# Kernel tuning notes

Hardware: AMD Instinct MI355X
Metric: run time of the kernel (lower is better)

Reference implementation:

```python
import jax, jax.numpy as jnp
import numpy as np
from jax import lax

C = 256          # fpn_feats_dim
NC = 20          # num_classes
GROUPS = 16      # GroupNorm groups
EPS = 1e-5       # GroupNorm eps (torch default)
BATCH = 8
LEVELS = [(100, 128), (50, 64), (25, 32)]  # FPN level H,W for 800x1024 image, strides 8/16/32
PRIOR_BIAS = -float(np.log((1 - 0.01) / 0.01))  # ~-4.5951, FCOS prior init


def _conv3(x, w, b):
    # 3x3 stride-1 pad-1 conv, NCHW / OIHW
    y = lax.conv_general_dilated(x, w, (1, 1), 'SAME',
                                 dimension_numbers=('NCHW', 'OIHW', 'NCHW'))
    return y + b[None, :, None, None]


def _gn(x, g, b):
    n, c, h, w = x.shape
    xr = x.reshape(n, GROUPS, c // GROUPS, h, w)
    m = xr.mean(axis=(2, 3, 4), keepdims=True)
    v = xr.var(axis=(2, 3, 4), keepdims=True)
    xr = (xr - m) * lax.rsqrt(v + EPS)
    x = xr.reshape(n, c, h, w)
    return x * g[None, :, None, None] + b[None, :, None, None]


def _forward(feat0, feat1, feat2,
             cls_conv_w, cls_conv_b, cls_gn_g, cls_gn_b, cls_out_w, cls_out_b,
             reg_conv_w, reg_conv_b, reg_gn_g, reg_gn_b,
             reg_out_w, reg_out_b, ctr_w, ctr_b):
    feats = [feat0, feat1, feat2]
    all_cls, all_reg, all_ctr = [], [], []
    for f in feats:
        n = f.shape[0]
        x = f
        for i in range(2):
            x = jax.nn.relu(_gn(_conv3(x, cls_conv_w[i], cls_conv_b[i]),
                                cls_gn_g[i], cls_gn_b[i]))
        logits = _conv3(x, cls_out_w, cls_out_b)           # [N, NC, H, W]
        # view(N,-1,NC,H,W).permute(0,3,4,1,2).reshape(N,-1,NC) == NHWC flatten
        all_cls.append(logits.transpose(0, 2, 3, 1).reshape(n, -1, NC))
        t = f
        for i in range(2):
            t = jax.nn.relu(_gn(_conv3(t, reg_conv_w[i], reg_conv_b[i]),
                                reg_gn_g[i], reg_gn_b[i]))
        # bbox_reg = Sequential(conv, ReLU), then an extra relu in forward (idempotent)
        bbox = jax.nn.relu(jax.nn.relu(_conv3(t, reg_out_w, reg_out_b)))  # [N,4,H,W]
        all_reg.append(bbox.transpose(0, 2, 3, 1).reshape(n, -1, 1))      # [N,H*W*4,1]
        ctr = _conv3(t, ctr_w, ctr_b)                                     # [N,1,H,W]
        all_ctr.append(ctr.transpose(0, 2, 3, 1).reshape(n, -1, 1))       # [N,H*W,1]
    cls_cat = jnp.concatenate(all_cls, axis=1)
    reg_cat = jnp.concatenate(all_reg, axis=1)
    ctr_cat = jnp.concatenate(all_ctr, axis=1)
    return cls_cat, reg_cat, ctr_cat


def setup_inputs() -> dict:
    key = jax.random.key(0)
    ks = jax.random.split(key, 20)
    std = 0.01
    d = {}
    for i, (h, w) in enumerate(LEVELS):
        d[f"feat{i}"] = jax.random.normal(ks[i], (BATCH, C, h, w), jnp.float32)
    # classification head params
    d["cls_conv_w"] = jax.random.normal(ks[3], (2, C, C, 3, 3), jnp.float32) * std
    d["cls_conv_b"] = jnp.zeros((2, C), jnp.float32)
    d["cls_gn_g"] = jnp.ones((2, C), jnp.float32)
    d["cls_gn_b"] = jnp.zeros((2, C), jnp.float32)
    d["cls_out_w"] = jax.random.normal(ks[4], (NC, C, 3, 3), jnp.float32) * std
    d["cls_out_b"] = jnp.full((NC,), PRIOR_BIAS, jnp.float32)
    d["reg_conv_w"] = jax.random.normal(ks[5], (2, C, C, 3, 3), jnp.float32) * std
    d["reg_conv_b"] = jnp.zeros((2, C), jnp.float32)
    d["reg_gn_g"] = jnp.ones((2, C), jnp.float32)
    d["reg_gn_b"] = jnp.zeros((2, C), jnp.float32)
    d["reg_out_w"] = jax.random.normal(ks[6], (4, C, 3, 3), jnp.float32) * std
    d["reg_out_b"] = jnp.zeros((4,), jnp.float32)
    d["ctr_w"] = jax.random.normal(ks[7], (1, C, 3, 3), jnp.float32) * std
    d["ctr_b"] = jnp.zeros((1,), jnp.float32)
    return d


def reference(feat0, feat1, feat2,
              cls_conv_w, cls_conv_b, cls_gn_g, cls_gn_b, cls_out_w, cls_out_b,
              reg_conv_w, reg_conv_b, reg_gn_g, reg_gn_b,
              reg_out_w, reg_out_b, ctr_w, ctr_b):
    return _forward(feat0, feat1, feat2,
                    cls_conv_w, cls_conv_b, cls_gn_g, cls_gn_b, cls_out_w, cls_out_b,
                    reg_conv_w, reg_conv_b, reg_gn_g, reg_gn_b,
                    reg_out_w, reg_out_b, ctr_w, ctr_b)
```

## Files before the change

kernel.cpp:

```cpp
#include <hip/hip_runtime.h>

typedef unsigned short u16;
typedef __attribute__((ext_vector_type(8))) unsigned short ushort8v;
typedef __attribute__((ext_vector_type(8))) short short8v;
typedef __attribute__((ext_vector_type(4))) float floatx4;

__device__ __forceinline__ float bf2f(u16 u) {
    unsigned v = ((unsigned)u) << 16;
    float f;
    __builtin_memcpy(&f, &v, 4);
    return f;
}
__device__ __forceinline__ u16 f2bf(float f) {
    unsigned v;
    __builtin_memcpy(&v, &f, 4);
    unsigned r = (v + 0x7fffu + ((v >> 16) & 1u)) >> 16;
    return (u16)r;
}
__device__ __forceinline__ float ld(const void* p, long i, int isf) {
    return isf ? ((const float*)p)[i] : bf2f(((const u16*)p)[i]);
}
__device__ __forceinline__ void gll16(const void* g, void* l) {
    __builtin_amdgcn_global_load_lds(
        (const __attribute__((address_space(1))) unsigned int*)g,
        (__attribute__((address_space(3))) unsigned int*)l, 16, 0, 0);
}

__global__ void detect_dtype(const u16* __restrict__ gng, int* __restrict__ flag) {
    if (threadIdx.x == 0) flag[0] = (gng[0] == 0x3F80u) ? 0 : 1;
}

__global__ void conv_params(const void* ccb, const void* cgg, const void* cgb,
                            const void* rcb, const void* rgg, const void* rgb,
                            const void* cob, const void* rob, const void* ctb,
                            const int* __restrict__ flag, u16* __restrict__ dst) {
    const int isf = flag[0];
    for (int i = threadIdx.x; i < 3104; i += 256) {
        const void* src; int off;
        if (i < 512)       { src = ccb; off = i; }
        else if (i < 1024) { src = cgg; off = i - 512; }
        else if (i < 1536) { src = cgb; off = i - 1024; }
        else if (i < 2048) { src = rcb; off = i - 1536; }
        else if (i < 2560) { src = rgg; off = i - 2048; }
        else if (i < 3072) { src = rgb; off = i - 2560; }
        else if (i < 3092) { src = cob; off = i - 3072; }
        else if (i < 3096) { src = rob; off = i - 3092; }
        else if (i < 3097) { src = ctb; off = 0; }
        else               { dst[i] = 0; continue; }
        dst[i] = f2bf(ld(src, off, isf));
    }
}

__global__ void prep_w(const void* __restrict__ src, long srcOff,
                       const int* __restrict__ flag, u16* __restrict__ dst,
                       int CoutSrc, int BNr) {
    const int isf = flag[0];
    unsigned e = blockIdx.x * 256 + threadIdx.x;
    unsigned c = e & 31u;
    unsigned r = (e >> 5) % (unsigned)BNr;
    unsigned kc = (e / (32u * BNr)) % 72u;
    unsigned nt = e / (32u * BNr * 72u);
    unsigned co = nt * BNr + r;
    unsigned tap = kc >> 3, ci = (kc & 7u) * 32u + c;
    u16 v = 0;
    if (co < (unsigned)CoutSrc)
        v = f2bf(ld(src, srcOff + (long)(co * 256u + ci) * 9 + tap, isf));
    dst[e] = v;
}

__global__ void prep_w_regctr(const void* __restrict__ wreg, const void* __restrict__ wctr,
                              const int* __restrict__ flag, u16* __restrict__ dst) {
    const int isf = flag[0];
    unsigned e = blockIdx.x * 256 + threadIdx.x;
    unsigned c = e & 31u;
    unsigned r = (e >> 5) & 31u;
    unsigned kc = e / 1024u;
    unsigned tap = kc >> 3, ci = (kc & 7u) * 32u + c;
    u16 v = 0;
    if (r < 4u)       v = f2bf(ld(wreg, (long)(r * 256u + ci) * 9 + tap, isf));
    else if (r == 4u) v = f2bf(ld(wctr, (long)ci * 9 + tap, isf));
    dst[e] = v;
}

__global__ void zero_border(u16* __restrict__ buf, int H, int Wp, int Hp, int NB) {
    const int nb = 2 * Wp + 2 * H;
    unsigned idx = blockIdx.x * 256 + threadIdx.x;
    unsigned ch = idx & 31u;
    unsigned rem = idx >> 5;
    unsigned n = rem / (unsigned)nb;
    unsigned b = rem - n * nb;
    if (n >= (unsigned)NB) return;
    int ppos;
    if ((int)b < Wp) ppos = (int)b;
    else if ((int)b < 2 * Wp) ppos = (Hp - 1) * Wp + ((int)b - Wp);
    else {
        int r = (int)b - 2 * Wp;
        ppos = (1 + (r >> 1)) * Wp + ((r & 1) ? (Wp - 1) : 0);
    }
    ushort8v z = {};
    *(ushort8v*)(buf + ((long)n * (Hp * Wp) + ppos) * 256 + ch * 8) = z;
}

__global__ void nchw_to_nhwc_pad(const void* __restrict__ src, long srcOff,
                                 const int* __restrict__ flag, u16* __restrict__ dst,
                                 int S, int W, int Wp, int HpWp) {
    const int isf = flag[0];
    __shared__ u16 t[64][34];
    const int tid = threadIdx.x;
    const int n = blockIdx.z, ct = blockIdx.y;
    const int s0 = blockIdx.x * 32;
    const long base = srcOff + ((long)(n * 256 + ct * 64)) * S + s0;
#pragma unroll
    for (int i = 0; i < 8; ++i) {
        int c = i * 8 + (tid >> 5);
        t[c][tid & 31] = f2bf(ld(src, base + (long)c * S + (tid & 31), isf));
    }
    __syncthreads();
#pragma unroll
    for (int i = 0; i < 8; ++i) {
        int px = i * 4 + (tid >> 6);
        int s = s0 + px;
        int y = s / W, x = s - y * W;
        dst[((long)n * HpWp + (long)(y + 1) * Wp + (x + 1)) * 256 + ct * 64 + (tid & 63)] =
            t[tid & 63][px];
    }
}

__global__ void gn_stats(const u16* __restrict__ x, float* __restrict__ stats, int S) {
    const int n = blockIdx.x >> 4, g = blockIdx.x & 15;
    const int tid = threadIdx.x;
    float sum = 0.f, sq = 0.f;
    const u16* base = x + (long)n * S * 256 + g * 16 + (tid & 7) * 2;
    for (int p = tid >> 3; p < S; p += 32) {
        unsigned v = *(const unsigned*)(base + (long)p * 256);
        float x0 = bf2f((u16)(v & 0xffffu));
        float x1 = bf2f((u16)(v >> 16));
        sum += x0 + x1;
        sq += x0 * x0 + x1 * x1;
    }
#pragma unroll
    for (int off = 32; off > 0; off >>= 1) {
        sum += __shfl_down(sum, off, 64);
        sq  += __shfl_down(sq, off, 64);
    }
    __shared__ float red[8];
    const int wave = tid >> 6, lane = tid & 63;
    if (lane == 0) { red[wave * 2] = sum; red[wave * 2 + 1] = sq; }
    __syncthreads();
    if (tid == 0) {
        stats[(n * 16 + g) * 2]     = red[0] + red[2] + red[4] + red[6];
        stats[(n * 16 + g) * 2 + 1] = red[1] + red[3] + red[5] + red[7];
    }
}

__global__ void gn_norm_relu(const u16* __restrict__ x, const float* __restrict__ stats,
                             const u16* __restrict__ gam, const u16* __restrict__ bet,
                             u16* __restrict__ outp, int S, int W, int Wp, int HpWp,
                             float invC) {
    unsigned idx = blockIdx.x * 256 + threadIdx.x;
    unsigned c8 = idx & 31u;
    unsigned rem = idx >> 5;
    unsigned p = rem % (unsigned)S;
    unsigned n = rem / (unsigned)S;
    unsigned c0 = c8 * 8u;
    unsigned g = c0 >> 4;
    float sum = stats[(n * 16 + g) * 2], sq = stats[(n * 16 + g) * 2 + 1];
    float mean = sum * invC;
    float var = fmaxf(sq * invC - mean * mean, 0.f);
    float rstd = rsqrtf(var + 1e-5f);
    ushort8v v = *(const ushort8v*)(x + ((long)(n * S + p)) * 256 + c0);
    unsigned y = p / (unsigned)W, xc = p - y * W;
    u16* dst = outp + ((long)n * HpWp + (long)(y + 1) * Wp + (xc + 1)) * 256 + c0;
    ushort8v o;
#pragma unroll
    for (int j = 0; j < 8; ++j) {
        float xv = bf2f(v[j]);
        float r = (xv - mean) * rstd * bf2f(gam[c0 + j]) + bf2f(bet[c0 + j]);
        o[j] = f2bf(fmaxf(r, 0.f));
    }
    *(ushort8v*)dst = o;
}

template <int BN, int MODE>
__global__ __launch_bounds__(256, 2)
void conv_gemm(const u16* __restrict__ Ap, const u16* __restrict__ Wb,
               const u16* __restrict__ bias, const u16* __restrict__ bias2,
               void* __restrict__ outp, long ob1, long ob2,
               const int* __restrict__ dflag,
               int M, int n0, int S, int W, int Wp, int HpWp, int prefS) {
    static_assert(BN == 256 || BN == 32, "");
    constexpr int MI = (BN == 256) ? 4 : 2;
    constexpr int NI = (BN == 256) ? 8 : 2;
    constexpr int ASZ = 128 * 32;
    constexpr int BSZ = BN * 32;
    __shared__ __align__(16) u16 ldsA[2 * ASZ];
    __shared__ __align__(16) u16 ldsB[2 * BSZ];
    const int tid = threadIdx.x;
    const int lane = tid & 63, wave = tid >> 6;

    const unsigned NTg = gridDim.y;
    const unsigned nwg = gridDim.x * NTg;
    const unsigned lin = blockIdx.y * gridDim.x + blockIdx.x;
    const unsigned qq = nwg >> 3, rr = nwg & 7u;
    const unsigned xcd = lin & 7u, pos = lin >> 3;
    const unsigned wg =
        (xcd < rr ? xcd * (qq + 1u) : rr * (qq + 1u) + (xcd - rr) * qq) + pos;
    const int nt = (int)(wg % NTg);
    const int m0 = (int)(wg / NTg) * 128;

    int isf = 0;
    if (MODE != 0) isf = dflag[0];

    const int r0 = 32 * wave + (lane >> 2);
    int mA0 = m0 + r0;        if (mA0 > M - 1) mA0 = M - 1;
    int mA1 = m0 + r0 + 16;   if (mA1 > M - 1) mA1 = M - 1;
    const char* aL0;
    const char* aL1;
    {
        int n8 = mA0 / S, s = mA0 - n8 * S, y = s / W, x = s - y * W;
        aL0 = (const char*)(Ap + ((long)n8 * HpWp + (long)(y + 1) * Wp + (x + 1)) * 256)
              + (lane & 3) * 16;
        n8 = mA1 / S; s = mA1 - n8 * S; y = s / W; x = s - y * W;
        aL1 = (const char*)(Ap + ((long)n8 * HpWp + (long)(y + 1) * Wp + (x + 1)) * 256)
              + (lane & 3) * 16;
    }
    u16* lA0 = ldsA + (32 * wave) * 32;
    u16* lA1 = ldsA + (32 * wave + 16) * 32;

    const u16* b_tile = Wb + (long)nt * 72 * BN * 32;
    const char* bsrc0;
    u16* lB0;
    if (BN == 256) {
        bsrc0 = (const char*)b_tile + (64 * wave) * 64 + lane * 16;
        lB0 = ldsB + (64 * wave) * 32;
    } else {
        bsrc0 = (const char*)b_tile + wave * 1024 + lane * 16;
        lB0 = ldsB + wave * 16 * 32;
    }

    auto STAGE = [&](int kc, int p) {
        const int tap = kc >> 3;
        const int ty = tap / 3;
        const int tx = tap - ty * 3;
        const long aoffB = (long)((ty - 1) * Wp + (tx - 1)) * 512 + (kc & 7) * 64;
        gll16(aL0 + aoffB, lA0 + p * ASZ);
        gll16(aL1 + aoffB, lA1 + p * ASZ);
        if (BN == 256) {
            const char* bs = bsrc0 + (long)kc * 16384;
            u16* lb = lB0 + p * BSZ;
            gll16(bs,        lb);
            gll16(bs + 1024, lb + 16 * 32);
            gll16(bs + 2048, lb + 32 * 32);
            gll16(bs + 3072, lb + 48 * 32);
        } else {
            if (wave < 2) gll16(bsrc0 + (long)kc * 2048, lB0 + p * BSZ);
        }
    };

    floatx4 acc[MI][NI] = {};

    const int wm = (BN == 256) ? (wave & 1) * 64 : wave * 32;
    const int wn = (BN == 256) ? (wave >> 1) * 128 : 0;
    const int fr = lane & 15, q = lane >> 4;
    const u16* fA = ldsA + (wm + fr) * 32 + q * 8;
    const u16* fB = ldsB + (wn + fr) * 32 + q * 8;

    STAGE(0, 0);
    asm volatile("s_waitcnt vmcnt(0)" ::: "memory");
    __builtin_amdgcn_s_barrier();

#pragma unroll 1
    for (int kc = 0; kc < 71; ++kc) {
        const int p = kc & 1;
        STAGE(kc + 1, p ^ 1);
        short8v af[MI], bf[NI];
        const u16* fAp = fA + p * ASZ;
        const u16* fBp = fB + p * BSZ;
#pragma unroll
        for (int i = 0; i < MI; ++i) af[i] = *(const short8v*)(fAp + i * 16 * 32);
#pragma unroll
        for (int j = 0; j < NI; ++j) bf[j] = *(const short8v*)(fBp + j * 16 * 32);
#pragma unroll
        for (int i = 0; i < MI; ++i)
#pragma unroll
            for (int j = 0; j < NI; ++j)
                acc[i][j] = __builtin_amdgcn_mfma_f32_16x16x32_bf16(af[i], bf[j],
                                                                    acc[i][j], 0, 0, 0);
        asm volatile("s_waitcnt vmcnt(0)" ::: "memory");
        __builtin_amdgcn_s_barrier();
    }
    {
        short8v af[MI], bf[NI];
        const u16* fAp = fA + ASZ;
        const u16* fBp = fB + BSZ;
#pragma unroll
        for (int i = 0; i < MI; ++i) af[i] = *(const short8v*)(fAp + i * 16 * 32);
#pragma unroll
        for (int j = 0; j < NI; ++j) bf[j] = *(const short8v*)(fBp + j * 16 * 32);
#pragma unroll
        for (int i = 0; i < MI; ++i)
#pragma unroll
            for (int j = 0; j < NI; ++j)
                acc[i][j] = __builtin_amdgcn_mfma_f32_16x16x32_bf16(af[i], bf[j],
                                                                    acc[i][j], 0, 0, 0);
    }

    if (MODE == 0) {
        u16* out = (u16*)outp;
#pragma unroll
        for (int j = 0; j < NI; ++j) {
            const int co = nt * BN + wn + j * 16 + fr;
            const float bv = bf2f(bias[co]);
#pragma unroll
            for (int i = 0; i < MI; ++i) {
#pragma unroll
                for (int r = 0; r < 4; ++r) {
                    const int mg = m0 + wm + i * 16 + q * 4 + r;
                    if (mg < M)
                        out[(long)mg * 256 + co] = f2bf(acc[i][j][r] + bv);
                }
            }
        }
    } else {
#pragma unroll
        for (int i = 0; i < MI; ++i) {
#pragma unroll
            for (int r = 0; r < 4; ++r) {
                const int mg = m0 + wm + i * 16 + q * 4 + r;
                if (mg >= M) continue;
                const int n8 = mg / S;
                const int s = mg - n8 * S;
                const long gi = n0 + n8;
#pragma unroll
                for (int j = 0; j < NI; ++j) {
                    const int co = wn + j * 16 + fr;
                    const float v = acc[i][j][r];
                    long oi = -1;
                    float val = 0.f;
                    if (MODE == 1) {
                        if (co < 20) {
                            oi = ob1 + gi * 336000 + (long)(prefS + s) * 20 + co;
                            val = v + bf2f(bias[co]);
                        }
                    } else {
                        if (co < 4) {
                            oi = ob1 + gi * 67200 + (long)(prefS + s) * 4 + co;
                            val = fmaxf(v + bf2f(bias[co]), 0.f);
                        } else if (co == 4) {
                            oi = ob2 + gi * 16800 + (prefS + s);
                            val = v + bf2f(bias2[0]);
                        }
                    }
                    if (oi >= 0) {
                        if (isf) ((float*)outp)[oi] = val;
                        else     ((u16*)outp)[oi] = f2bf(val);
                    }
                }
            }
        }
    }
}

extern "C" void kernel_launch(void* const* d_in, const int* in_sizes, int n_in,
                              void* d_out, int out_size, void* d_ws, size_t ws_size,
                              hipStream_t stream) {
    (void)in_sizes; (void)n_in; (void)out_size;
    const void* feat[3]   = {d_in[0], d_in[1], d_in[2]};
    const void* cls_conv_w = d_in[3];
    const void* cls_conv_b = d_in[4];
    const void* cls_gn_g   = d_in[5];
    const void* cls_gn_b   = d_in[6];
    const void* cls_out_w  = d_in[7];
    const void* cls_out_b  = d_in[8];
    const void* reg_conv_w = d_in[9];
    const void* reg_conv_b = d_in[10];
    const void* reg_gn_g   = d_in[11];
    const void* reg_gn_b   = d_in[12];
    const void* reg_out_w  = d_in[13];
    const void* reg_out_b  = d_in[14];
    const void* ctr_w      = d_in[15];
    const void* ctr_b      = d_in[16];

    char* ws = (char*)d_ws;
    int*  flag     = (int*)ws;
    u16*  params   = (u16*)(ws + 1024);
    u16*  Wb       = (u16*)(ws + 8192);
    float* stats   = (float*)(ws + 5021696);
    const size_t base = 5022720;
    const size_t per_img = 6789120ull + 6553600ull + 6789120ull;
    int NB = 8;
    while (NB > 1 && base + (size_t)NB * per_img > ws_size) NB >>= 1;
    u16* feat_pad  = (u16*)(ws + base);
    u16* conv_out  = (u16*)(ws + base + (size_t)NB * 6789120ull);
    u16* norm_pad  = (u16*)(ws + base + (size_t)NB * (6789120ull + 6553600ull));

    detect_dtype<<<1, 64, 0, stream>>>((const u16*)cls_gn_g, flag);
    conv_params<<<1, 256, 0, stream>>>(cls_conv_b, cls_gn_g, cls_gn_b,
                                       reg_conv_b, reg_gn_g, reg_gn_b,
                                       cls_out_b, reg_out_b, ctr_b, flag, params);
    prep_w<<<2304, 256, 0, stream>>>(cls_conv_w, 0,      flag, Wb + 0,       256, 256);
    prep_w<<<2304, 256, 0, stream>>>(cls_conv_w, 589824, flag, Wb + 589824,  256, 256);
    prep_w<<<2304, 256, 0, stream>>>(reg_conv_w, 0,      flag, Wb + 1179648, 256, 256);
    prep_w<<<2304, 256, 0, stream>>>(reg_conv_w, 589824, flag, Wb + 1769472, 256, 256);
    prep_w<<<288,  256, 0, stream>>>(cls_out_w,  0,      flag, Wb + 2359296, 20, 32);
    prep_w_regctr<<<288, 256, 0, stream>>>(reg_out_w, ctr_w, flag, Wb + 2433024);

    const int Hs[3] = {100, 50, 25}, Wss[3] = {128, 64, 32};
    const int prefSs[3] = {0, 12800, 16000};

    for (int l = 0; l < 3; ++l) {
        const int H = Hs[l], W = Wss[l], S = H * W;
        const int Hp = H + 2, Wp = W + 2, HpWp = Hp * Wp;
        const int prefS = prefSs[l];
        const int nb = 2 * Wp + 2 * H;
        const float invC = 1.0f / (16.0f * (float)S);

        for (int n0 = 0; n0 < 8; n0 += NB) {
            const int M = NB * S;
            const int mtiles = (M + 127) / 128;
            const int zb_blocks = (NB * nb * 32 + 255) / 256;

            zero_border<<<zb_blocks, 256, 0, stream>>>(feat_pad, H, Wp, Hp, NB);
            zero_border<<<zb_blocks, 256, 0, stream>>>(norm_pad, H, Wp, Hp, NB);
            nchw_to_nhwc_pad<<<dim3(S / 32, 4, NB), 256, 0, stream>>>(
                feat[l], (long)n0 * 256 * S, flag, feat_pad, S, W, Wp, HpWp);

            conv_gemm<256, 0><<<dim3(mtiles, 1), 256, 0, stream>>>(
                feat_pad, Wb + 0, params + 0, nullptr, conv_out, 0, 0, flag,
                M, n0, S, W, Wp, HpWp, 0);
            gn_stats<<<NB * 16, 256, 0, stream>>>(conv_out, stats, S);
            gn_norm_relu<<<M / 8, 256, 0, stream>>>(conv_out, stats, params + 512,
                                                    params + 1024, norm_pad,
                                                    S, W, Wp, HpWp, invC);
            conv_gemm<256, 0><<<dim3(mtiles, 1), 256, 0, stream>>>(
                norm_pad, Wb + 589824, params + 256, nullptr, conv_out, 0, 0, flag,
                M, n0, S, W, Wp, HpWp, 0);
            gn_stats<<<NB * 16, 256, 0, stream>>>(conv_out, stats, S);
            gn_norm_relu<<<M / 8, 256, 0, stream>>>(conv_out, stats, params + 512 + 256,
                                                    params + 1024 + 256, norm_pad,
                                                    S, W, Wp, HpWp, invC);
            conv_gemm<32, 1><<<dim3(mtiles, 1), 256, 0, stream>>>(
                norm_pad, Wb + 2359296, params + 3072, nullptr, d_out, 0, 0, flag,
                M, n0, S, W, Wp, HpWp, prefS);

            conv_gemm<256, 0><<<dim3(mtiles, 1), 256, 0, stream>>>(
                feat_pad, Wb + 1179648, params + 1536, nullptr, conv_out, 0, 0, flag,
                M, n0, S, W, Wp, HpWp, 0);
            gn_stats<<<NB * 16, 256, 0, stream>>>(conv_out, stats, S);
            gn_norm_relu<<<M / 8, 256, 0, stream>>>(conv_out, stats, params + 2048,
                                                    params + 2560, norm_pad,
                                                    S, W, Wp, HpWp, invC);
            conv_gemm<256, 0><<<dim3(mtiles, 1), 256, 0, stream>>>(
                norm_pad, Wb + 1769472, params + 1536 + 256, nullptr, conv_out, 0, 0, flag,
                M, n0, S, W, Wp, HpWp, 0);
            gn_stats<<<NB * 16, 256, 0, stream>>>(conv_out, stats, S);
            gn_norm_relu<<<M / 8, 256, 0, stream>>>(conv_out, stats, params + 2048 + 256,
                                                    params + 2560 + 256, norm_pad,
                                                    S, W, Wp, HpWp, invC);
            conv_gemm<32, 2><<<dim3(mtiles, 1), 256, 0, stream>>>(
                norm_pad, Wb + 2433024, params + 3092, params + 3096,
                d_out, 2688000, 3225600, flag,
                M, n0, S, W, Wp, HpWp, prefS);
        }
    }
}
```

Before: 2.767 ms.

## Triple-buffer conv GEMM LDS staging and XOR-swizzle LDS layout

Moves the implicit-GEMM conv main loop from double to triple buffering with partial vmcnt waits, so global-to-LDS loads run two K-chunks ahead instead of draining every iteration. It also XOR-swizzles the 16-byte chunk position within each 64-byte LDS row, on both the load and fragment-read sides, to reduce LDS bank conflicts. LDS use grows by half, which can lower occupancy at launch_bounds(256,2). An extra barrier is added per iteration to protect buffer reuse.

```diff
diff --git a/kernel.cpp b/kernel.cpp
--- a/kernel.cpp
+++ b/kernel.cpp
@@ -193,8 +193,8 @@
     constexpr int NI = (BN == 256) ? 8 : 2;
     constexpr int ASZ = 128 * 32;
     constexpr int BSZ = BN * 32;
-    __shared__ __align__(16) u16 ldsA[2 * ASZ];
-    __shared__ __align__(16) u16 ldsB[2 * BSZ];
+    __shared__ __align__(16) u16 ldsA[3 * ASZ];
+    __shared__ __align__(16) u16 ldsB[3 * BSZ];
     const int tid = threadIdx.x;
     const int lane = tid & 63, wave = tid >> 6;
 
@@ -211,6 +211,8 @@
     int isf = 0;
     if (MODE != 0) isf = dflag[0];
 
+    const int csw = ((lane & 3) ^ ((lane >> 2) & 3)) * 16;
+
     const int r0 = 32 * wave + (lane >> 2);
     int mA0 = m0 + r0;        if (mA0 > M - 1) mA0 = M - 1;
     int mA1 = m0 + r0 + 16;   if (mA1 > M - 1) mA1 = M - 1;
@@ -219,10 +221,10 @@
     {
         int n8 = mA0 / S, s = mA0 - n8 * S, y = s / W, x = s - y * W;
         aL0 = (const char*)(Ap + ((long)n8 * HpWp + (long)(y + 1) * Wp + (x + 1)) * 256)
-              + (lane & 3) * 16;
+              + csw;
         n8 = mA1 / S; s = mA1 - n8 * S; y = s / W; x = s - y * W;
         aL1 = (const char*)(Ap + ((long)n8 * HpWp + (long)(y + 1) * Wp + (x + 1)) * 256)
-              + (lane & 3) * 16;
+              + csw;
     }
     u16* lA0 = ldsA + (32 * wave) * 32;
     u16* lA1 = ldsA + (32 * wave + 16) * 32;
@@ -231,10 +233,10 @@
     const char* bsrc0;
     u16* lB0;
     if (BN == 256) {
-        bsrc0 = (const char*)b_tile + (64 * wave) * 64 + lane * 16;
+        bsrc0 = (const char*)b_tile + (64 * wave + (lane >> 2)) * 64 + csw;
         lB0 = ldsB + (64 * wave) * 32;
     } else {
-        bsrc0 = (const char*)b_tile + wave * 1024 + lane * 16;
+        bsrc0 = (const char*)b_tile + (16 * wave + (lane >> 2)) * 64 + csw;
         lB0 = ldsB + wave * 16 * 32;
     }
 
@@ -262,17 +264,22 @@
     const int wm = (BN == 256) ? (wave & 1) * 64 : wave * 32;
     const int wn = (BN == 256) ? (wave >> 1) * 128 : 0;
     const int fr = lane & 15, q = lane >> 4;
-    const u16* fA = ldsA + (wm + fr) * 32 + q * 8;
-    const u16* fB = ldsB + (wn + fr) * 32 + q * 8;
+    const int qs = (q ^ (fr & 3)) * 8;
+    const u16* fA = ldsA + (wm + fr) * 32 + qs;
+    const u16* fB = ldsB + (wn + fr) * 32 + qs;
 
     STAGE(0, 0);
-    asm volatile("s_waitcnt vmcnt(0)" ::: "memory");
-    __builtin_amdgcn_s_barrier();
-
+    STAGE(1, 1);
+    STAGE(2, 2);
+
+    int p = 0;
 #pragma unroll 1
-    for (int kc = 0; kc < 71; ++kc) {
-        const int p = kc & 1;
-        STAGE(kc + 1, p ^ 1);
+    for (int kc = 0; kc < 70; ++kc) {
+        if constexpr (BN == 256)
+            asm volatile("s_waitcnt vmcnt(12)" ::: "memory");
+        else
+            asm volatile("s_waitcnt vmcnt(4)" ::: "memory");
+        __builtin_amdgcn_s_barrier();
         short8v af[MI], bf[NI];
         const u16* fAp = fA + p * ASZ;
         const u16* fBp = fB + p * BSZ;
@@ -280,19 +287,43 @@
         for (int i = 0; i < MI; ++i) af[i] = *(const short8v*)(fAp + i * 16 * 32);
 #pragma unroll
         for (int j = 0; j < NI; ++j) bf[j] = *(const short8v*)(fBp + j * 16 * 32);
+        asm volatile("s_waitcnt lgkmcnt(0)" ::: "memory");
+        __builtin_amdgcn_s_barrier();
+        if (kc < 69) STAGE(kc + 3, p);
 #pragma unroll
         for (int i = 0; i < MI; ++i)
 #pragma unroll
             for (int j = 0; j < NI; ++j)
                 acc[i][j] = __builtin_amdgcn_mfma_f32_16x16x32_bf16(af[i], bf[j],
                                                                     acc[i][j], 0, 0, 0);
+        p = (p == 2) ? 0 : p + 1;
+    }
+    {
+        if constexpr (BN == 256)
+            asm volatile("s_waitcnt vmcnt(6)" ::: "memory");
+        else
+            asm volatile("s_waitcnt vmcnt(2)" ::: "memory");
+        __builtin_amdgcn_s_barrier();
+        short8v af[MI], bf[NI];
+        const u16* fAp = fA + 1 * ASZ;
+        const u16* fBp = fB + 1 * BSZ;
+#pragma unroll
+        for (int i = 0; i < MI; ++i) af[i] = *(const short8v*)(fAp + i * 16 * 32);
+#pragma unroll
+        for (int j = 0; j < NI; ++j) bf[j] = *(const short8v*)(fBp + j * 16 * 32);
+#pragma unroll
+        for (int i = 0; i < MI; ++i)
+#pragma unroll
+            for (int j = 0; j < NI; ++j)
+                acc[i][j] = __builtin_amdgcn_mfma_f32_16x16x32_bf16(af[i], bf[j],
+                                                                    acc[i][j], 0, 0, 0);
+    }
+    {
         asm volatile("s_waitcnt vmcnt(0)" ::: "memory");
         __builtin_amdgcn_s_barrier();
-    }
-    {
         short8v af[MI], bf[NI];
-        const u16* fAp = fA + ASZ;
-        const u16* fBp = fB + BSZ;
+        const u16* fAp = fA + 2 * ASZ;
+        const u16* fBp = fB + 2 * BSZ;
 #pragma unroll
         for (int i = 0; i < MI; ++i) af[i] = *(const short8v*)(fAp + i * 16 * 32);
 #pragma unroll
```

New measurement: 2.315 ms. 1.2x faster.
